# Optimization experiments

Measured on AMD Instinct MI355X. Metric: run time of the kernel, lower is better.

Reference implementation:

```python
import jax, jax.numpy as jnp
import numpy as np

D_MODEL = 1024
NUM_HEADS = 16
DEPTH = D_MODEL // NUM_HEADS


def setup_inputs() -> dict:
    key = jax.random.key(0)
    ks = jax.random.split(key, 9)
    B, S = 2, 2048
    scale = 1.0 / np.sqrt(D_MODEL)
    inputs = jax.random.normal(ks[0], (B, S, D_MODEL), dtype=jnp.float32)
    wq = jax.random.normal(ks[1], (D_MODEL, D_MODEL), dtype=jnp.float32) * scale
    wk = jax.random.normal(ks[2], (D_MODEL, D_MODEL), dtype=jnp.float32) * scale
    wv = jax.random.normal(ks[3], (D_MODEL, D_MODEL), dtype=jnp.float32) * scale
    wo = jax.random.normal(ks[4], (D_MODEL, D_MODEL), dtype=jnp.float32) * scale
    bq = jnp.zeros((D_MODEL,), jnp.float32)
    bk = jnp.zeros((D_MODEL,), jnp.float32)
    bv = jnp.zeros((D_MODEL,), jnp.float32)
    bo = jnp.zeros((D_MODEL,), jnp.float32)
    return {"inputs": inputs, "wq": wq, "bq": bq, "wk": wk, "bk": bk,
            "wv": wv, "bv": bv, "wo": wo, "bo": bo}


def _split_heads(x):
    # [B, S, D] -> [B, H, S, depth]
    B, S, _ = x.shape
    return x.reshape(B, S, NUM_HEADS, DEPTH).transpose(0, 2, 1, 3)


def reference(inputs, wq, bq, wk, bk, wv, bv, wo, bo):
    B, S, _ = inputs.shape
    q = _split_heads(inputs @ wq + bq)   # [B,H,S,d]
    k = _split_heads(inputs @ wk + bk)
    v = _split_heads(inputs @ wv + bv)
    scale = 1.0 / jnp.sqrt(jnp.float32(DEPTH))
    logits = jnp.einsum('bhqd,bhkd->bhqk', q, k) * scale  # [B,H,S,S]
    attn = jax.nn.softmax(logits, axis=-1)
    # dropout is identity at inference time
    out = jnp.einsum('bhqk,bhkd->bhqd', attn, v)          # [B,H,S,d]
    out = out.transpose(0, 2, 1, 3).reshape(B, S, D_MODEL)
    return out @ wo + bo
```

## Files before the change

### kernel.cpp

```cpp
#include <hip/hip_runtime.h>
#include <cstdint>
#include <cstddef>

#define D_MODEL 1024
#define S_LEN   2048
#define NHEAD   16
#define DHEAD   64
#define BSZ     2
#define LOG2E   1.44269504088896f

typedef short  short8  __attribute__((ext_vector_type(8)));
typedef float  floatx4 __attribute__((ext_vector_type(4)));
typedef unsigned short u16x4 __attribute__((ext_vector_type(4)));

__device__ inline unsigned short f2b(float f) {
  union { float f; unsigned int u; } v; v.f = f;
  unsigned int r = v.u + 0x7FFFu + ((v.u >> 16) & 1u);
  return (unsigned short)(r >> 16);
}

__device__ inline void gload_lds16(const void* g, void* l) {
  __builtin_amdgcn_global_load_lds(
      (const __attribute__((address_space(1))) unsigned int*)g,
      (__attribute__((address_space(3))) unsigned int*)l, 16, 0, 0);
}

__global__ __launch_bounds__(256) void k_prep(
    const float* __restrict__ x,
    const float* __restrict__ wq, const float* __restrict__ wk,
    const float* __restrict__ wv, const float* __restrict__ wo,
    unsigned short* __restrict__ xb, unsigned short* __restrict__ wqkvT,
    unsigned short* __restrict__ woT) {
  int bid = blockIdx.x;
  if (bid < 4096) {
    int i = bid * 256 + threadIdx.x;
    float4 f = ((const float4*)x)[i];
    u16x4 o;
    o[0] = f2b(f.x); o[1] = f2b(f.y); o[2] = f2b(f.z); o[3] = f2b(f.w);
    ((u16x4*)xb)[i] = o;
    return;
  }
  __shared__ float tile[32][33];
  int r = bid - 4096;
  int which = r >> 10, tl = r & 1023;
  const float* src = (which == 0) ? wq : (which == 1) ? wk : (which == 2) ? wv : wo;
  unsigned short* dst = (which < 3) ? (wqkvT + (size_t)which * 1024 * 1024) : woT;
  int bx = (tl & 31) * 32;
  int by = (tl >> 5) * 32;
  int tx = threadIdx.x & 31, ty0 = threadIdx.x >> 5;
  #pragma unroll
  for (int i = 0; i < 4; i++) {
    int ty = ty0 + i * 8;
    tile[ty][tx] = src[(size_t)(by + ty) * D_MODEL + bx + tx];
  }
  __syncthreads();
  #pragma unroll
  for (int i = 0; i < 4; i++) {
    int ty = ty0 + i * 8;
    dst[(size_t)(bx + ty) * D_MODEL + by + tx] = f2b(tile[tx][ty]);
  }
}

__device__ inline void gemm_tiles(const unsigned short* __restrict__ A,
                                  const unsigned short* __restrict__ Bt,
                                  int m0, int n0, short* As, short* Bs,
                                  floatx4 acc[4][4]) {
  const int t = threadIdx.x, w = t >> 6, lane = t & 63;
  const int wr = w >> 1, wc = w & 1, g = lane >> 4, l15 = lane & 15;
  floatx4 zf = {0.f, 0.f, 0.f, 0.f};
  #pragma unroll
  for (int m = 0; m < 4; m++)
    #pragma unroll
    for (int n = 0; n < 4; n++) acc[m][n] = zf;

  auto stage = [&](int kt, int b) {
    #pragma unroll
    for (int i = 0; i < 2; i++) {
      int p = i * 256 + t;
      int row = p >> 2, ce = (p & 3) << 3;
      gload_lds16(A  + (size_t)(m0 + row) * D_MODEL + kt * 32 + ce,
                  (char*)As + b * 8192 + i * 4096 + w * 1024);
      gload_lds16(Bt + (size_t)(n0 + row) * D_MODEL + kt * 32 + ce,
                  (char*)Bs + b * 8192 + i * 4096 + w * 1024);
    }
  };

  stage(0, 0);
  __syncthreads();
  #pragma unroll 2
  for (int kt = 0; kt < D_MODEL / 32; kt++) {
    int b = kt & 1;
    if (kt < D_MODEL / 32 - 1) stage(kt + 1, b ^ 1);

    short8 af[4], bfr[4];
    #pragma unroll
    for (int m = 0; m < 4; m++)
      af[m] = *(const short8*)((const char*)As + b * 8192 + (wr * 64 + m * 16 + l15) * 64 + g * 16);
    #pragma unroll
    for (int n = 0; n < 4; n++)
      bfr[n] = *(const short8*)((const char*)Bs + b * 8192 + (wc * 64 + n * 16 + l15) * 64 + g * 16);
    __builtin_amdgcn_s_setprio(1);
    #pragma unroll
    for (int m = 0; m < 4; m++)
      #pragma unroll
      for (int n = 0; n < 4; n++)
        acc[m][n] = __builtin_amdgcn_mfma_f32_16x16x32_bf16(af[m], bfr[n], acc[m][n], 0, 0, 0);
    __builtin_amdgcn_s_setprio(0);
    __syncthreads();
  }
}

__global__ __launch_bounds__(256) void k_gemm_qkv(
    const unsigned short* __restrict__ xb, const unsigned short* __restrict__ wT,
    const float* __restrict__ bq, const float* __restrict__ bk, const float* __restrict__ bv,
    unsigned short* __restrict__ qb, unsigned short* __restrict__ kb,
    unsigned short* __restrict__ vb) {
  __shared__ __align__(16) short As[8192], Bs[8192];
  floatx4 acc[4][4];
  int m0 = blockIdx.y * 128, n0 = blockIdx.x * 128;
  gemm_tiles(xb, wT, m0, n0, As, Bs, acc);
  int t = threadIdx.x, w = t >> 6, lane = t & 63;
  int wr = w >> 1, wc = w & 1, g = lane >> 4, l15 = lane & 15;
  #pragma unroll
  for (int m = 0; m < 4; m++) {
    #pragma unroll
    for (int n = 0; n < 4; n++) {
      #pragma unroll
      for (int j = 0; j < 4; j++) {
        int row = m0 + wr * 64 + m * 16 + g * 4 + j;
        int col = n0 + wc * 64 + n * 16 + l15;
        int sel = col >> 10, c = col & 1023;
        float bias = (sel == 0) ? bq[c] : (sel == 1) ? bk[c] : bv[c];
        float v = acc[m][n][j] + bias;
        if (sel == 0) v *= 0.125f * LOG2E;
        unsigned short* dst = (sel == 0) ? qb : (sel == 1) ? kb : vb;
        int h = c >> 6, dd = c & 63;
        int b_ = row >> 11, ss = row & 2047;
        dst[(size_t)((b_ * NHEAD + h) * S_LEN + ss) * DHEAD + dd] = f2b(v);
      }
    }
  }
}

__global__ __launch_bounds__(256) void k_tv(const unsigned short* __restrict__ V,
                                            unsigned short* __restrict__ Vt) {
  __shared__ unsigned short tile[64][72];
  int bh = blockIdx.y, s0 = blockIdx.x * 64;
  int t = threadIdx.x;
  int c = (t & 15) << 2;
  int r0 = t >> 4;
  const unsigned short* src = V + (size_t)(bh * S_LEN + s0) * DHEAD;
  #pragma unroll
  for (int i = 0; i < 4; i++) {
    int r = r0 + i * 16;
    *(u16x4*)&tile[r][c] = *(const u16x4*)(src + (size_t)r * DHEAD + c);
  }
  __syncthreads();
  unsigned short* dstb = Vt + (size_t)bh * DHEAD * S_LEN + s0;
  #pragma unroll
  for (int i = 0; i < 4; i++) {
    int d = r0 + i * 16;
    u16x4 o;
    o[0] = tile[c + 0][d]; o[1] = tile[c + 1][d];
    o[2] = tile[c + 2][d]; o[3] = tile[c + 3][d];
    *(u16x4*)(dstb + (size_t)d * S_LEN + c) = o;
  }
}

__global__ __launch_bounds__(128) void k_attn(
    const unsigned short* __restrict__ Q, const unsigned short* __restrict__ K,
    const unsigned short* __restrict__ Vt, unsigned short* __restrict__ O) {
  __shared__ __align__(16) char Ks[2][8192], Vs[2][8192], Ps[8192];
  int qt = blockIdx.x, bh = blockIdx.y;
  int t = threadIdx.x, w = t >> 6, lane = t & 63, g = lane >> 4, l15 = lane & 15;
  const unsigned short* Qh = Q + (size_t)bh * S_LEN * DHEAD;
  const unsigned short* Kh = K + (size_t)bh * S_LEN * DHEAD;
  const unsigned short* Vh = Vt + (size_t)bh * DHEAD * S_LEN;
  int q0 = qt * 64;

  #pragma unroll
  for (int i = 0; i < 4; i++) {
    int p = i * 128 + t;
    int row = p >> 3;
    int sb = ((p & 7) << 4) ^ ((row & 7) << 4);
    gload_lds16(Qh + (size_t)(q0 + row) * DHEAD + (sb >> 1), Ps    + i * 2048 + w * 1024);
    gload_lds16(Kh + (size_t)row * DHEAD + (sb >> 1),        Ks[0] + i * 2048 + w * 1024);
    gload_lds16(Vh + (size_t)row * S_LEN + (sb >> 1),        Vs[0] + i * 2048 + w * 1024);
  }
  __syncthreads();

  const int lxor = (l15 & 7) << 4;
  short8 qf[2][2];
  #pragma unroll
  for (int qg = 0; qg < 2; qg++)
    #pragma unroll
    for (int ks = 0; ks < 2; ks++) {
      int row = w * 32 + qg * 16 + l15;
      qf[qg][ks] = *(const short8*)(Ps + row * 128 + ((ks * 64 + g * 16) ^ lxor));
    }

  short8 onesf;
  #pragma unroll
  for (int i = 0; i < 8; i++) onesf[i] = (short)0x3F80;

  floatx4 o[2][5];
  floatx4 zf = {0.f, 0.f, 0.f, 0.f};
  #pragma unroll
  for (int qg = 0; qg < 2; qg++)
    #pragma unroll
    for (int n = 0; n < 5; n++) o[qg][n] = zf;

  char* Pw = Ps + w * 4096;

  #pragma unroll 2
  for (int kt = 0; kt < S_LEN / 64; kt++) {
    int b = kt & 1;
    if (kt < S_LEN / 64 - 1) {
      #pragma unroll
      for (int i = 0; i < 4; i++) {
        int p = i * 128 + t;
        int row = p >> 3;
        int sb = ((p & 7) << 4) ^ ((row & 7) << 4);
        gload_lds16(Kh + (size_t)((kt + 1) * 64 + row) * DHEAD + (sb >> 1),
                    Ks[b ^ 1] + i * 2048 + w * 1024);
        gload_lds16(Vh + (size_t)row * S_LEN + (kt + 1) * 64 + (sb >> 1),
                    Vs[b ^ 1] + i * 2048 + w * 1024);
      }
    }

    floatx4 s[2][4];
    #pragma unroll
    for (int qg = 0; qg < 2; qg++)
      #pragma unroll
      for (int n = 0; n < 4; n++) s[qg][n] = zf;
    __builtin_amdgcn_s_setprio(1);
    #pragma unroll
    for (int ks = 0; ks < 2; ks++) {
      #pragma unroll
      for (int n = 0; n < 4; n++) {
        int row = n * 16 + l15;
        short8 kf = *(const short8*)(Ks[b] + row * 128 + ((ks * 64 + g * 16) ^ lxor));
        s[0][n] = __builtin_amdgcn_mfma_f32_16x16x32_bf16(qf[0][ks], kf, s[0][n], 0, 0, 0);
        s[1][n] = __builtin_amdgcn_mfma_f32_16x16x32_bf16(qf[1][ks], kf, s[1][n], 0, 0, 0);
      }
    }
    __builtin_amdgcn_s_setprio(0);

    #pragma unroll
    for (int qg = 0; qg < 2; qg++) {
      #pragma unroll
      for (int n = 0; n < 4; n++) {
        #pragma unroll
        for (int j = 0; j < 4; j++) {
          int row = qg * 16 + g * 4 + j;
          int cb = ((n * 16 + l15) * 2) ^ (((g * 4 + j) & 7) << 4);
          *(unsigned short*)(Pw + row * 128 + cb) =
              f2b(__builtin_amdgcn_exp2f(s[qg][n][j]));
        }
      }
    }
    __asm__ volatile("s_waitcnt lgkmcnt(0)" ::: "memory");
    __builtin_amdgcn_sched_barrier(0);

    __builtin_amdgcn_s_setprio(1);
    #pragma unroll
    for (int ks = 0; ks < 2; ks++) {
      short8 pa0 = *(const short8*)(Pw + (l15)      * 128 + ((ks * 64 + g * 16) ^ lxor));
      short8 pa1 = *(const short8*)(Pw + (16 + l15) * 128 + ((ks * 64 + g * 16) ^ lxor));
      #pragma unroll
      for (int n = 0; n < 4; n++) {
        int vr = n * 16 + l15;
        short8 vf = *(const short8*)(Vs[b] + vr * 128 + ((ks * 64 + g * 16) ^ lxor));
        o[0][n] = __builtin_amdgcn_mfma_f32_16x16x32_bf16(pa0, vf, o[0][n], 0, 0, 0);
        o[1][n] = __builtin_amdgcn_mfma_f32_16x16x32_bf16(pa1, vf, o[1][n], 0, 0, 0);
      }
      o[0][4] = __builtin_amdgcn_mfma_f32_16x16x32_bf16(pa0, onesf, o[0][4], 0, 0, 0);
      o[1][4] = __builtin_amdgcn_mfma_f32_16x16x32_bf16(pa1, onesf, o[1][4], 0, 0, 0);
    }
    __builtin_amdgcn_s_setprio(0);
    __syncthreads();
  }

  int b_ = bh >> 4, h = bh & 15;
  #pragma unroll
  for (int qg = 0; qg < 2; qg++) {
    float inv[4];
    #pragma unroll
    for (int j = 0; j < 4; j++) inv[j] = 1.0f / o[qg][4][j];
    #pragma unroll
    for (int n = 0; n < 4; n++) {
      #pragma unroll
      for (int j = 0; j < 4; j++) {
        int row = q0 + w * 32 + qg * 16 + g * 4 + j;
        int col = h * 64 + n * 16 + l15;
        O[(size_t)(b_ * S_LEN + row) * D_MODEL + col] = f2b(o[qg][n][j] * inv[j]);
      }
    }
  }
}

__global__ __launch_bounds__(256) void k_gemm_out(
    const unsigned short* __restrict__ ab, const unsigned short* __restrict__ woT,
    const float* __restrict__ bo, float* __restrict__ out) {
  __shared__ __align__(16) short As[2][2048], Bs[2][4096];
  const int t = threadIdx.x, w = t >> 6, lane = t & 63;
  const int g = lane >> 4, l15 = lane & 15;
  int m0 = blockIdx.y * 64, n0 = blockIdx.x * 128;
  floatx4 acc[4][2];
  floatx4 zf = {0.f, 0.f, 0.f, 0.f};
  #pragma unroll
  for (int m = 0; m < 4; m++) { acc[m][0] = zf; acc[m][1] = zf; }

  auto stage = [&](int kt, int b) {
    {
      int row = t >> 2, ce = (t & 3) << 3;
      gload_lds16(ab + (size_t)(m0 + row) * D_MODEL + kt * 32 + ce,
                  (char*)As[b] + w * 1024);
    }
    #pragma unroll
    for (int i = 0; i < 2; i++) {
      int p = i * 256 + t;
      int row = p >> 2, ce = (p & 3) << 3;
      gload_lds16(woT + (size_t)(n0 + row) * D_MODEL + kt * 32 + ce,
                  (char*)Bs[b] + i * 4096 + w * 1024);
    }
  };

  stage(0, 0);
  __syncthreads();
  #pragma unroll 2
  for (int kt = 0; kt < D_MODEL / 32; kt++) {
    int b = kt & 1;
    if (kt < D_MODEL / 32 - 1) stage(kt + 1, b ^ 1);
    short8 af[4], bfr[2];
    #pragma unroll
    for (int m = 0; m < 4; m++)
      af[m] = *(const short8*)((const char*)As[b] + (m * 16 + l15) * 64 + g * 16);
    #pragma unroll
    for (int n = 0; n < 2; n++)
      bfr[n] = *(const short8*)((const char*)Bs[b] + (w * 32 + n * 16 + l15) * 64 + g * 16);
    __builtin_amdgcn_s_setprio(1);
    #pragma unroll
    for (int m = 0; m < 4; m++)
      #pragma unroll
      for (int n = 0; n < 2; n++)
        acc[m][n] = __builtin_amdgcn_mfma_f32_16x16x32_bf16(af[m], bfr[n], acc[m][n], 0, 0, 0);
    __builtin_amdgcn_s_setprio(0);
    __syncthreads();
  }

  #pragma unroll
  for (int m = 0; m < 4; m++) {
    #pragma unroll
    for (int n = 0; n < 2; n++) {
      #pragma unroll
      for (int j = 0; j < 4; j++) {
        int row = m0 + m * 16 + g * 4 + j;
        int col = n0 + w * 32 + n * 16 + l15;
        out[(size_t)row * D_MODEL + col] = acc[m][n][j] + bo[col];
      }
    }
  }
}

extern "C" void kernel_launch(void* const* d_in, const int* in_sizes, int n_in,
                              void* d_out, int out_size, void* d_ws, size_t ws_size,
                              hipStream_t stream) {
  const float* x  = (const float*)d_in[0];
  const float* wq = (const float*)d_in[1];
  const float* bq = (const float*)d_in[2];
  const float* wk = (const float*)d_in[3];
  const float* bk = (const float*)d_in[4];
  const float* wv = (const float*)d_in[5];
  const float* bv = (const float*)d_in[6];
  const float* wo = (const float*)d_in[7];
  const float* bo = (const float*)d_in[8];
  float* out = (float*)d_out;

  char* ws = (char*)d_ws;
  unsigned short* xb    = (unsigned short*)(ws);
  unsigned short* wqkvT = (unsigned short*)(ws + 8388608);
  unsigned short* woT   = (unsigned short*)(ws + 14680064);
  unsigned short* qb    = (unsigned short*)(ws + 16777216);
  unsigned short* kb    = (unsigned short*)(ws + 25165824);
  unsigned short* vb    = (unsigned short*)(ws + 33554432);
  unsigned short* vtb   = (unsigned short*)(ws + 41943040);
  unsigned short* ab    = xb;

  k_prep<<<8192, 256, 0, stream>>>(x, wq, wk, wv, wo, xb, wqkvT, woT);
  k_gemm_qkv<<<dim3(24, 32), 256, 0, stream>>>(xb, wqkvT, bq, bk, bv, qb, kb, vb);
  k_tv<<<dim3(32, 32), 256, 0, stream>>>(vb, vtb);
  k_attn<<<dim3(32, 32), 128, 0, stream>>>(qb, kb, vtb, ab);
  k_gemm_out<<<dim3(8, 64), 256, 0, stream>>>(ab, woT, bo, out);
}
```

Measured before the change: 224.0 us.

## Fuse V transpose into QKV GEMM and rewrite attention with 32x32 MFMA in registers

```diff
diff --git a/kernel.cpp b/kernel.cpp
--- a/kernel.cpp
+++ b/kernel.cpp
@@ -9,8 +9,9 @@
 #define BSZ     2
 #define LOG2E   1.44269504088896f
 
-typedef short  short8  __attribute__((ext_vector_type(8)));
-typedef float  floatx4 __attribute__((ext_vector_type(4)));
+typedef short  short8   __attribute__((ext_vector_type(8)));
+typedef float  floatx4  __attribute__((ext_vector_type(4)));
+typedef float  floatx16 __attribute__((ext_vector_type(16)));
 typedef unsigned short u16x4 __attribute__((ext_vector_type(4)));
 
 __device__ inline unsigned short f2b(float f) {
@@ -114,7 +115,7 @@
     const unsigned short* __restrict__ xb, const unsigned short* __restrict__ wT,
     const float* __restrict__ bq, const float* __restrict__ bk, const float* __restrict__ bv,
     unsigned short* __restrict__ qb, unsigned short* __restrict__ kb,
-    unsigned short* __restrict__ vb) {
+    unsigned short* __restrict__ vtb) {
   __shared__ __align__(16) short As[8192], Bs[8192];
   floatx4 acc[4][4];
   int m0 = blockIdx.y * 128, n0 = blockIdx.x * 128;
@@ -125,54 +126,44 @@
   for (int m = 0; m < 4; m++) {
     #pragma unroll
     for (int n = 0; n < 4; n++) {
-      #pragma unroll
-      for (int j = 0; j < 4; j++) {
-        int row = m0 + wr * 64 + m * 16 + g * 4 + j;
-        int col = n0 + wc * 64 + n * 16 + l15;
-        int sel = col >> 10, c = col & 1023;
-        float bias = (sel == 0) ? bq[c] : (sel == 1) ? bk[c] : bv[c];
-        float v = acc[m][n][j] + bias;
-        if (sel == 0) v *= 0.125f * LOG2E;
-        unsigned short* dst = (sel == 0) ? qb : (sel == 1) ? kb : vb;
-        int h = c >> 6, dd = c & 63;
-        int b_ = row >> 11, ss = row & 2047;
-        dst[(size_t)((b_ * NHEAD + h) * S_LEN + ss) * DHEAD + dd] = f2b(v);
-      }
-    }
-  }
-}
-
-__global__ __launch_bounds__(256) void k_tv(const unsigned short* __restrict__ V,
-                                            unsigned short* __restrict__ Vt) {
-  __shared__ unsigned short tile[64][72];
-  int bh = blockIdx.y, s0 = blockIdx.x * 64;
-  int t = threadIdx.x;
-  int c = (t & 15) << 2;
-  int r0 = t >> 4;
-  const unsigned short* src = V + (size_t)(bh * S_LEN + s0) * DHEAD;
-  #pragma unroll
-  for (int i = 0; i < 4; i++) {
-    int r = r0 + i * 16;
-    *(u16x4*)&tile[r][c] = *(const u16x4*)(src + (size_t)r * DHEAD + c);
-  }
-  __syncthreads();
-  unsigned short* dstb = Vt + (size_t)bh * DHEAD * S_LEN + s0;
-  #pragma unroll
-  for (int i = 0; i < 4; i++) {
-    int d = r0 + i * 16;
-    u16x4 o;
-    o[0] = tile[c + 0][d]; o[1] = tile[c + 1][d];
-    o[2] = tile[c + 2][d]; o[3] = tile[c + 3][d];
-    *(u16x4*)(dstb + (size_t)d * S_LEN + c) = o;
+      int row0 = m0 + wr * 64 + m * 16 + g * 4;
+      int col  = n0 + wc * 64 + n * 16 + l15;
+      int sel = col >> 10, c = col & 1023;
+      int h = c >> 6, dd = c & 63;
+      int b_ = row0 >> 11, ss = row0 & 2047;
+      if (sel == 2) {
+        u16x4 o;
+        #pragma unroll
+        for (int j = 0; j < 4; j++) o[j] = f2b(acc[m][n][j] + bv[c]);
+        *(u16x4*)(vtb + ((size_t)(b_ * NHEAD + h) * DHEAD + dd) * S_LEN + ss) = o;
+      } else {
+        const float* bias = (sel == 0) ? bq : bk;
+        unsigned short* dst = (sel == 0) ? qb : kb;
+        float sc = (sel == 0) ? 0.125f * LOG2E : 1.0f;
+        #pragma unroll
+        for (int j = 0; j < 4; j++) {
+          float v = (acc[m][n][j] + bias[c]) * sc;
+          dst[(size_t)((b_ * NHEAD + h) * S_LEN + ss + j) * DHEAD + dd] = f2b(v);
+        }
+      }
+    }
   }
 }
 
 __global__ __launch_bounds__(128) void k_attn(
     const unsigned short* __restrict__ Q, const unsigned short* __restrict__ K,
     const unsigned short* __restrict__ Vt, unsigned short* __restrict__ O) {
-  __shared__ __align__(16) char Ks[2][8192], Vs[2][8192], Ps[8192];
-  int qt = blockIdx.x, bh = blockIdx.y;
-  int t = threadIdx.x, w = t >> 6, lane = t & 63, g = lane >> 4, l15 = lane & 15;
+  __shared__ __align__(16) char lds[32768];
+  char* KsB0 = lds;
+  char* KsB1 = lds + 8192;
+  char* VsB0 = lds + 16384;
+  char* VsB1 = lds + 24576;
+
+  int L = blockIdx.x;
+  int bh = (L & 7) + 8 * ((L >> 3) >> 5);
+  int qt = (L >> 3) & 31;
+
+  int t = threadIdx.x, w = t >> 6, lane = t & 63, l31 = lane & 31, hi = lane >> 5;
   const unsigned short* Qh = Q + (size_t)bh * S_LEN * DHEAD;
   const unsigned short* Kh = K + (size_t)bh * S_LEN * DHEAD;
   const unsigned short* Vh = Vt + (size_t)bh * DHEAD * S_LEN;
@@ -183,118 +174,107 @@
     int p = i * 128 + t;
     int row = p >> 3;
     int sb = ((p & 7) << 4) ^ ((row & 7) << 4);
-    gload_lds16(Qh + (size_t)(q0 + row) * DHEAD + (sb >> 1), Ps    + i * 2048 + w * 1024);
-    gload_lds16(Kh + (size_t)row * DHEAD + (sb >> 1),        Ks[0] + i * 2048 + w * 1024);
-    gload_lds16(Vh + (size_t)row * S_LEN + (sb >> 1),        Vs[0] + i * 2048 + w * 1024);
-  }
-  __syncthreads();
-
-  const int lxor = (l15 & 7) << 4;
-  short8 qf[2][2];
-  #pragma unroll
-  for (int qg = 0; qg < 2; qg++)
-    #pragma unroll
-    for (int ks = 0; ks < 2; ks++) {
-      int row = w * 32 + qg * 16 + l15;
-      qf[qg][ks] = *(const short8*)(Ps + row * 128 + ((ks * 64 + g * 16) ^ lxor));
-    }
-
-  short8 onesf;
-  #pragma unroll
-  for (int i = 0; i < 8; i++) onesf[i] = (short)0x3F80;
-
-  floatx4 o[2][5];
-  floatx4 zf = {0.f, 0.f, 0.f, 0.f};
-  #pragma unroll
-  for (int qg = 0; qg < 2; qg++)
-    #pragma unroll
-    for (int n = 0; n < 5; n++) o[qg][n] = zf;
-
-  char* Pw = Ps + w * 4096;
+    gload_lds16(Qh + (size_t)(q0 + row) * DHEAD + (sb >> 1), VsB1 + i * 2048 + w * 1024);
+    gload_lds16(Kh + (size_t)row * DHEAD + (sb >> 1),        KsB0 + i * 2048 + w * 1024);
+    gload_lds16(Vh + (size_t)row * S_LEN + (sb >> 1),        VsB0 + i * 2048 + w * 1024);
+  }
+  __syncthreads();
+
+  const int swz = (l31 & 7) << 4;
+  short8 qf[4];
+  #pragma unroll
+  for (int ds = 0; ds < 4; ds++)
+    qf[ds] = *(const short8*)(VsB1 + (w * 32 + l31) * 128 + ((32 * ds + 16 * hi) ^ swz));
+  __asm__ volatile("s_waitcnt lgkmcnt(0)" ::: "memory");
+  __syncthreads();
+
+  floatx16 accd[2];
+  #pragma unroll
+  for (int dt = 0; dt < 2; dt++)
+    #pragma unroll
+    for (int r = 0; r < 16; r++) accd[dt][r] = 0.f;
+  float lsum = 0.f;
 
   #pragma unroll 2
   for (int kt = 0; kt < S_LEN / 64; kt++) {
     int b = kt & 1;
+    char* Ks = b ? KsB1 : KsB0;
+    char* Vs = b ? VsB1 : VsB0;
     if (kt < S_LEN / 64 - 1) {
+      char* Kn = b ? KsB0 : KsB1;
+      char* Vn = b ? VsB0 : VsB1;
       #pragma unroll
       for (int i = 0; i < 4; i++) {
         int p = i * 128 + t;
         int row = p >> 3;
         int sb = ((p & 7) << 4) ^ ((row & 7) << 4);
-        gload_lds16(Kh + (size_t)((kt + 1) * 64 + row) * DHEAD + (sb >> 1),
-                    Ks[b ^ 1] + i * 2048 + w * 1024);
-        gload_lds16(Vh + (size_t)row * S_LEN + (kt + 1) * 64 + (sb >> 1),
-                    Vs[b ^ 1] + i * 2048 + w * 1024);
-      }
-    }
-
-    floatx4 s[2][4];
-    #pragma unroll
-    for (int qg = 0; qg < 2; qg++)
-      #pragma unroll
-      for (int n = 0; n < 4; n++) s[qg][n] = zf;
-    __builtin_amdgcn_s_setprio(1);
-    #pragma unroll
-    for (int ks = 0; ks < 2; ks++) {
-      #pragma unroll
-      for (int n = 0; n < 4; n++) {
-        int row = n * 16 + l15;
-        short8 kf = *(const short8*)(Ks[b] + row * 128 + ((ks * 64 + g * 16) ^ lxor));
-        s[0][n] = __builtin_amdgcn_mfma_f32_16x16x32_bf16(qf[0][ks], kf, s[0][n], 0, 0, 0);
-        s[1][n] = __builtin_amdgcn_mfma_f32_16x16x32_bf16(qf[1][ks], kf, s[1][n], 0, 0, 0);
-      }
-    }
-    __builtin_amdgcn_s_setprio(0);
-
-    #pragma unroll
-    for (int qg = 0; qg < 2; qg++) {
-      #pragma unroll
-      for (int n = 0; n < 4; n++) {
+        gload_lds16(Kh + (size_t)((kt + 1) * 64 + row) * DHEAD + (sb >> 1), Kn + i * 2048 + w * 1024);
+        gload_lds16(Vh + (size_t)row * S_LEN + (kt + 1) * 64 + (sb >> 1),   Vn + i * 2048 + w * 1024);
+      }
+    }
+
+    #pragma unroll
+    for (int kvt = 0; kvt < 2; kvt++) {
+      short8 kf[4];
+      #pragma unroll
+      for (int ds = 0; ds < 4; ds++)
+        kf[ds] = *(const short8*)(Ks + (kvt * 32 + l31) * 128 + ((32 * ds + 16 * hi) ^ swz));
+      floatx16 s;
+      #pragma unroll
+      for (int r = 0; r < 16; r++) s[r] = 0.f;
+      __builtin_amdgcn_s_setprio(1);
+      #pragma unroll
+      for (int ds = 0; ds < 4; ds++)
+        s = __builtin_amdgcn_mfma_f32_32x32x16_bf16(kf[ds], qf[ds], s, 0, 0, 0);
+      __builtin_amdgcn_s_setprio(0);
+
+      float p[16];
+      #pragma unroll
+      for (int r = 0; r < 16; r++) { p[r] = __builtin_amdgcn_exp2f(s[r]); lsum += p[r]; }
+      unsigned int pk0[4], pk1[4];
+      #pragma unroll
+      for (int m = 0; m < 4; m++) {
+        __asm__("v_cvt_pk_bf16_f32 %0, %1, %2" : "=v"(pk0[m]) : "v"(p[4 * m + 0]), "v"(p[4 * m + 1]));
+        __asm__("v_cvt_pk_bf16_f32 %0, %1, %2" : "=v"(pk1[m]) : "v"(p[4 * m + 2]), "v"(p[4 * m + 3]));
+      }
+      short8 pf[2];
+      #pragma unroll
+      for (int ks = 0; ks < 2; ks++) {
+        unsigned int a0 = pk0[2 * ks], a1 = pk1[2 * ks];
+        unsigned int b0 = pk0[2 * ks + 1], b1 = pk1[2 * ks + 1];
+        __asm__("v_permlane32_swap_b32 %0, %1" : "+v"(a0), "+v"(b0));
+        __asm__("v_permlane32_swap_b32 %0, %1" : "+v"(a1), "+v"(b1));
+        union { unsigned int u[4]; short8 s8; } fu;
+        fu.u[0] = a0; fu.u[1] = a1; fu.u[2] = b0; fu.u[3] = b1;
+        pf[ks] = fu.s8;
+      }
+
+      __builtin_amdgcn_s_setprio(1);
+      #pragma unroll
+      for (int ks = 0; ks < 2; ks++) {
+        int slice = kvt * 2 + ks;
         #pragma unroll
-        for (int j = 0; j < 4; j++) {
-          int row = qg * 16 + g * 4 + j;
-          int cb = ((n * 16 + l15) * 2) ^ (((g * 4 + j) & 7) << 4);
-          *(unsigned short*)(Pw + row * 128 + cb) =
-              f2b(__builtin_amdgcn_exp2f(s[qg][n][j]));
+        for (int dt = 0; dt < 2; dt++) {
+          short8 vf = *(const short8*)(Vs + (dt * 32 + l31) * 128 + ((32 * slice + 16 * hi) ^ swz));
+          accd[dt] = __builtin_amdgcn_mfma_f32_32x32x16_bf16(vf, pf[ks], accd[dt], 0, 0, 0);
         }
       }
-    }
-    __asm__ volatile("s_waitcnt lgkmcnt(0)" ::: "memory");
-    __builtin_amdgcn_sched_barrier(0);
-
-    __builtin_amdgcn_s_setprio(1);
-    #pragma unroll
-    for (int ks = 0; ks < 2; ks++) {
-      short8 pa0 = *(const short8*)(Pw + (l15)      * 128 + ((ks * 64 + g * 16) ^ lxor));
-      short8 pa1 = *(const short8*)(Pw + (16 + l15) * 128 + ((ks * 64 + g * 16) ^ lxor));
-      #pragma unroll
-      for (int n = 0; n < 4; n++) {
-        int vr = n * 16 + l15;
-        short8 vf = *(const short8*)(Vs[b] + vr * 128 + ((ks * 64 + g * 16) ^ lxor));
-        o[0][n] = __builtin_amdgcn_mfma_f32_16x16x32_bf16(pa0, vf, o[0][n], 0, 0, 0);
-        o[1][n] = __builtin_amdgcn_mfma_f32_16x16x32_bf16(pa1, vf, o[1][n], 0, 0, 0);
-      }
-      o[0][4] = __builtin_amdgcn_mfma_f32_16x16x32_bf16(pa0, onesf, o[0][4], 0, 0, 0);
-      o[1][4] = __builtin_amdgcn_mfma_f32_16x16x32_bf16(pa1, onesf, o[1][4], 0, 0, 0);
-    }
-    __builtin_amdgcn_s_setprio(0);
+      __builtin_amdgcn_s_setprio(0);
+    }
     __syncthreads();
   }
 
+  float lfull = lsum + __shfl_xor(lsum, 32);
+  float inv = 1.0f / lfull;
   int b_ = bh >> 4, h = bh & 15;
-  #pragma unroll
-  for (int qg = 0; qg < 2; qg++) {
-    float inv[4];
-    #pragma unroll
-    for (int j = 0; j < 4; j++) inv[j] = 1.0f / o[qg][4][j];
-    #pragma unroll
-    for (int n = 0; n < 4; n++) {
-      #pragma unroll
-      for (int j = 0; j < 4; j++) {
-        int row = q0 + w * 32 + qg * 16 + g * 4 + j;
-        int col = h * 64 + n * 16 + l15;
-        O[(size_t)(b_ * S_LEN + row) * D_MODEL + col] = f2b(o[qg][n][j] * inv[j]);
-      }
+  int q = q0 + w * 32 + l31;
+  unsigned short* Orow = O + (size_t)(b_ * S_LEN + q) * D_MODEL + h * 64;
+  #pragma unroll
+  for (int dt = 0; dt < 2; dt++) {
+    #pragma unroll
+    for (int r = 0; r < 16; r++) {
+      int d = dt * 32 + (r & 3) + 8 * (r >> 2) + 4 * hi;
+      Orow[d] = f2b(accd[dt][r] * inv);
     }
   }
 }
@@ -383,13 +363,11 @@
   unsigned short* woT   = (unsigned short*)(ws + 14680064);
   unsigned short* qb    = (unsigned short*)(ws + 16777216);
   unsigned short* kb    = (unsigned short*)(ws + 25165824);
-  unsigned short* vb    = (unsigned short*)(ws + 33554432);
-  unsigned short* vtb   = (unsigned short*)(ws + 41943040);
+  unsigned short* vtb   = (unsigned short*)(ws + 33554432);
   unsigned short* ab    = xb;
 
   k_prep<<<8192, 256, 0, stream>>>(x, wq, wk, wv, wo, xb, wqkvT, woT);
-  k_gemm_qkv<<<dim3(24, 32), 256, 0, stream>>>(xb, wqkvT, bq, bk, bv, qb, kb, vb);
-  k_tv<<<dim3(32, 32), 256, 0, stream>>>(vb, vtb);
-  k_attn<<<dim3(32, 32), 128, 0, stream>>>(qb, kb, vtb, ab);
+  k_gemm_qkv<<<dim3(24, 32), 256, 0, stream>>>(xb, wqkvT, bq, bk, bv, qb, kb, vtb);
+  k_attn<<<1024, 128, 0, stream>>>(qb, kb, vtb, ab);
   k_gemm_out<<<dim3(8, 64), 256, 0, stream>>>(ab, woT, bo, out);
 }
```

Measured after the change: 221.2 us. Within noise of the previous version (-1.2%).
